# Kernel tuning notes

Measured on AMD Instinct MI355X. Metric: run time of the kernel, lower is better.

The kernel has to match this reference:

```python
import jax, jax.numpy as jnp
import numpy as np

TEMPERATURE = 0.07


def _unit(k, shape):
    x = jax.random.normal(k, shape, dtype=jnp.float32)
    return x / jnp.linalg.norm(x, axis=-1, keepdims=True)


def setup_inputs() -> dict:
    key = jax.random.key(0)
    ks = jax.random.split(key, 7)
    B, Cml, Cmc, D = 8192, 2048, 1000, 512
    features = _unit(ks[0], (B, D))
    ml_text = _unit(ks[1], (Cml, D))
    mc_text = _unit(ks[2], (Cmc, D))
    multilabel_targets = (jax.random.uniform(ks[3], (B, Cml)) < 0.05).astype(jnp.float32)
    # one-hot multiclass targets
    mc_idx = jax.random.randint(ks[4], (B,), 0, Cmc)
    multiclass_targets = jax.nn.one_hot(mc_idx, Cmc, dtype=jnp.float32)
    dataset_indices = jax.random.randint(ks[5], (B,), 0, 2).astype(jnp.int32)
    ratios = jax.random.uniform(ks[6], (Cml,), minval=0.05, maxval=0.95, dtype=jnp.float32)
    return {
        "features": features,
        "multilabel_text_features": ml_text,
        "multiclass_text_features": mc_text,
        "multilabel_targets": multilabel_targets,
        "multiclass_targets": multiclass_targets,
        "dataset_indices": dataset_indices,
        "ratios": ratios,
    }


def iterate_M(sim_matrix, b, num_iterations=2):
    # sim_matrix: [B, C, 2]; b: [C, 2]
    P = jnp.exp(sim_matrix)
    for _ in range(num_iterations):
        P = P / P.sum(axis=2, keepdims=True)          # row (last-dim) normalize
        P = P / (P.sum(axis=0) / b)                   # column normalize to marginals b
    return P


def iterate_P(sim_matrix, m, num_iterations=5):
    # sim_matrix: [B, C]
    P = jnp.exp(sim_matrix)
    for _ in range(num_iterations):
        row_sums = P.sum(axis=1)
        P = P / jnp.maximum(row_sums, 1.0)[:, None]
        P = P * m / P.sum()
    return P


def reference(features, multilabel_text_features, multiclass_text_features,
              multilabel_targets, multiclass_targets, dataset_indices, ratios):
    ml_sim = features @ multilabel_text_features.T / TEMPERATURE   # [B, Cml]
    mc_sim = features @ multiclass_text_features.T / TEMPERATURE   # [B, Cmc]

    n_mc = jnp.sum(dataset_indices == 1).astype(jnp.float32)
    n_ml = jnp.sum(dataset_indices == 0).astype(jnp.float32)
    m = n_mc + n_ml * 0.1

    P = iterate_P(mc_sim, m, 5)

    bs = ml_sim.shape[0]
    sim3 = jnp.stack([ml_sim / 2, -ml_sim / 2], axis=-1)           # [B, Cml, 2]
    b = jnp.stack([ratios, 1.0 - ratios], axis=1) * bs             # [Cml, 2]
    M = iterate_M(sim3, b, 2)

    ml_targets_final = jnp.stack([multilabel_targets, 1.0 - multilabel_targets], axis=-1)
    multilabel_loss = -jnp.sum(ml_targets_final * jnp.log(M)) * 0.5
    multiclass_loss = -jnp.sum(multiclass_targets * jnp.log(P))
    total_loss = multiclass_loss + multilabel_loss
    return total_loss
```

## Files before the change

kernel.cpp:

```cpp
#include <hip/hip_runtime.h>

typedef unsigned short u16;
typedef float f32x4 __attribute__((ext_vector_type(4)));
typedef short s16x8 __attribute__((ext_vector_type(8)));

#define GPTR(x) ((const __attribute__((address_space(1))) void*)(x))
#define LPTR(x) ((__attribute__((address_space(3))) void*)(x))

__device__ __forceinline__ u16 f32_to_bf16(float f) {
  unsigned u = __builtin_bit_cast(unsigned, f);
  u += 0x7FFFu + ((u >> 16) & 1u);
  return (u16)(u >> 16);
}
__device__ __forceinline__ float bf16_to_f32(u16 h) {
  unsigned u = ((unsigned)h) << 16;
  return __builtin_bit_cast(float, u);
}

__global__ __launch_bounds__(256) void k_cvt_all(
    const float* __restrict__ A, const float* __restrict__ ML, const float* __restrict__ MC,
    u16* __restrict__ Abf, u16* __restrict__ Bbf)
{
  int i = blockIdx.x * 256 + threadIdx.x;
  const float* src; u16* dst; int idx;
  bool pad = false;
  if (i < 1048576) { src = A; dst = Abf; idx = i; }
  else {
    int j = i - 1048576;
    if (j >= 393216) return;
    int row = j >> 7;
    dst = Bbf; idx = j;
    if (row < 2048) { src = ML; }
    else {
      int mcrow = row - 2048;
      src = MC; idx = j - 2048 * 128;
      pad = (mcrow >= 1000);
    }
  }
  ushort4 o = {0, 0, 0, 0};
  if (!pad) {
    float4 v = reinterpret_cast<const float4*>(src)[idx];
    o.x = f32_to_bf16(v.x); o.y = f32_to_bf16(v.y);
    o.z = f32_to_bf16(v.z); o.w = f32_to_bf16(v.w);
  }
  reinterpret_cast<ushort4*>(dst)[idx] = o;
}

__global__ __launch_bounds__(512) void k_gemm_fused(
    const u16* __restrict__ A, const u16* __restrict__ B,
    u16* __restrict__ Sml, float* __restrict__ colpart, float* __restrict__ pexp,
    float scale)
{
  constexpr int K = 512;
  constexpr int BK = 64;
  __shared__ __align__(16) u16 As[2][128 * BK];
  __shared__ __align__(16) u16 Bs[2][128 * BK];
  __shared__ float sred[128 * 4];

  const int tid  = threadIdx.x;
  const int lane = tid & 63;
  const int wave = tid >> 6;
  const int wr = wave >> 2;
  const int wc = wave & 3;

  int wg = (blockIdx.x & 7) * 192 + (blockIdx.x >> 3);
  const int bm = wg / 24;
  const int bn = wg % 24;
  const int row0 = bm * 128;
  const int col0 = bn * 128;
  const bool is_ml = (bn < 16);

  const int cr = (lane >> 4) * 4;
  const int cc = lane & 15;

  if (tid < 128) sred[tid] = 0.f;

  f32x4 acc[4][2];
#pragma unroll
  for (int i = 0; i < 4; ++i)
#pragma unroll
    for (int j = 0; j < 2; ++j) acc[i][j] = (f32x4){0.f, 0.f, 0.f, 0.f};

  auto stage = [&](int buf, int k0) {
#pragma unroll
    for (int q = 0; q < 2; ++q) {
      int base = wave * 128 + q * 64;
      int slot = base + lane;
      int r = slot >> 3, s = slot & 7;
      int sg = s ^ (r & 7);
      __builtin_amdgcn_global_load_lds(GPTR(A + (size_t)(row0 + r) * K + k0 + sg * 8),
                                       LPTR(&As[buf][base * 8]), 16, 0, 0);
      __builtin_amdgcn_global_load_lds(GPTR(B + (size_t)(col0 + r) * K + k0 + sg * 8),
                                       LPTR(&Bs[buf][base * 8]), 16, 0, 0);
    }
  };

  stage(0, 0);
  for (int t = 0; t < 8; ++t) {
    const int cur = t & 1;
    __syncthreads();
    if (t < 7) stage(cur ^ 1, (t + 1) * BK);
#pragma unroll
    for (int ks = 0; ks < 2; ++ks) {
      s16x8 af[4], bf[2];
#pragma unroll
      for (int mm = 0; mm < 4; ++mm) {
        int r = wr * 64 + mm * 16 + (lane & 15);
        int ss = (ks * 4 + (lane >> 4)) ^ (r & 7);
        af[mm] = *reinterpret_cast<const s16x8*>(&As[cur][r * BK + ss * 8]);
      }
#pragma unroll
      for (int nn = 0; nn < 2; ++nn) {
        int r = wc * 32 + nn * 16 + (lane & 15);
        int ss = (ks * 4 + (lane >> 4)) ^ (r & 7);
        bf[nn] = *reinterpret_cast<const s16x8*>(&Bs[cur][r * BK + ss * 8]);
      }
      __builtin_amdgcn_s_setprio(1);
#pragma unroll
      for (int mm = 0; mm < 4; ++mm)
#pragma unroll
        for (int nn = 0; nn < 2; ++nn)
          acc[mm][nn] = __builtin_amdgcn_mfma_f32_16x16x32_bf16(af[mm], bf[nn], acc[mm][nn], 0, 0, 0);
      __builtin_amdgcn_s_setprio(0);
    }
  }

  if (is_ml) {
#pragma unroll
    for (int mm = 0; mm < 4; ++mm) {
      int orow = row0 + wr * 64 + mm * 16 + cr;
#pragma unroll
      for (int nn = 0; nn < 2; ++nn) {
        int ocol = col0 + wc * 32 + nn * 16 + cc;
#pragma unroll
        for (int r = 0; r < 4; ++r)
          Sml[(size_t)(orow + r) * 2048 + ocol] = f32_to_bf16(acc[mm][nn][r] * scale);
      }
    }
    __syncthreads();
#pragma unroll
    for (int nn = 0; nn < 2; ++nn) {
      float cs = 0.f;
#pragma unroll
      for (int mm = 0; mm < 4; ++mm)
#pragma unroll
        for (int r = 0; r < 4; ++r) {
          float s = acc[mm][nn][r] * scale;
          cs += 1.f / (1.f + __expf(-s));
        }
      cs += __shfl_xor(cs, 16);
      cs += __shfl_xor(cs, 32);
      if (lane < 16) atomicAdd(&sred[wc * 32 + nn * 16 + lane], cs);
    }
    __syncthreads();
    if (tid < 128) colpart[(size_t)bm * 2048 + col0 + tid] = sred[tid];
  } else {
    const int mccol0 = col0 - 2048;
    float ex[16];
#pragma unroll
    for (int mm = 0; mm < 4; ++mm)
#pragma unroll
      for (int r = 0; r < 4; ++r) {
        float e = 0.f;
#pragma unroll
        for (int nn = 0; nn < 2; ++nn) {
          int ocol = mccol0 + wc * 32 + nn * 16 + cc;
          float s = acc[mm][nn][r] * scale;
          if (ocol < 1000) e += __expf(s);
        }
        ex[mm * 4 + r] = e;
      }
#pragma unroll
    for (int o = 1; o < 16; o <<= 1)
#pragma unroll
      for (int q = 0; q < 16; ++q) ex[q] += __shfl_xor(ex[q], o);
    __syncthreads();
    if ((lane & 15) == 0) {
#pragma unroll
      for (int mm = 0; mm < 4; ++mm)
#pragma unroll
        for (int r = 0; r < 4; ++r) {
          int lrow = wr * 64 + mm * 16 + cr + r;
          sred[lrow * 4 + wc] = ex[mm * 4 + r];
        }
    }
    __syncthreads();
    if (tid < 128) {
      size_t o = (size_t)(bn - 16) * 8192 + row0 + tid;
      pexp[o] = sred[tid * 4] + sred[tid * 4 + 1] + sred[tid * 4 + 2] + sred[tid * 4 + 3];
    }
  }
}

__global__ __launch_bounds__(256) void k_misc(
    const float* __restrict__ part, const float* __restrict__ ratios, float* __restrict__ c,
    const float* __restrict__ T2, const u16* __restrict__ A, const u16* __restrict__ B,
    float* __restrict__ rowdot, const float* __restrict__ pexp, float* __restrict__ Rbuf,
    float scale)
{
  if (blockIdx.x < 8) {
    int j = blockIdx.x * 256 + threadIdx.x;
    float s = 0.f;
    for (int ch = 0; ch < 64; ++ch) s += part[ch * 2048 + j];
    float b0 = ratios[j] * 8192.f;
    float b1 = (1.f - ratios[j]) * 8192.f;
    c[2 * j]     = b0 / s;
    c[2 * j + 1] = b1 / (8192.f - s);
    return;
  }
  if (blockIdx.x >= 2056) {
    int i = (blockIdx.x - 2056) * 256 + threadIdx.x;
    float e = 0.f;
#pragma unroll
    for (int ch = 0; ch < 8; ++ch) e += pexp[(size_t)ch * 8192 + i];
    Rbuf[i] = e;
    return;
  }
  int wave = threadIdx.x >> 6, lane = threadIdx.x & 63;
  int row = (blockIdx.x - 8) * 4 + wave;
  const float4* t4 = reinterpret_cast<const float4*>(T2 + (size_t)row * 1000);
  int idx = -1;
#pragma unroll
  for (int g = 0; g < 4; ++g) {
    int j4 = lane + g * 64;
    if (j4 < 250) {
      float4 v = t4[j4];
      if (v.x > 0.5f) idx = j4 * 4;
      if (v.y > 0.5f) idx = j4 * 4 + 1;
      if (v.z > 0.5f) idx = j4 * 4 + 2;
      if (v.w > 0.5f) idx = j4 * 4 + 3;
    }
  }
#pragma unroll
  for (int o = 32; o; o >>= 1) idx = max(idx, __shfl_xor(idx, o));

  s16x8 va = *reinterpret_cast<const s16x8*>(A + (size_t)row * 512 + lane * 8);
  s16x8 vb = *reinterpret_cast<const s16x8*>(B + (size_t)(2048 + idx) * 512 + lane * 8);
  float d = 0.f;
#pragma unroll
  for (int k = 0; k < 8; ++k)
    d += bf16_to_f32((u16)va[k]) * bf16_to_f32((u16)vb[k]);
#pragma unroll
  for (int o = 32; o; o >>= 1) d += __shfl_xor(d, o);
  if (lane == 0) rowdot[row] = d * scale;
}

__global__ __launch_bounds__(256) void k_ml_pass2(
    const u16* __restrict__ S, const float* __restrict__ T, const float* __restrict__ c,
    float* __restrict__ part2, float* __restrict__ partT, float* __restrict__ partE)
{
  const int t = threadIdx.x;
  const int r0 = blockIdx.x * 8;
  float c0[8], c1[8];
#pragma unroll
  for (int q = 0; q < 4; ++q) {
    float4 cv = reinterpret_cast<const float4*>(c)[t * 4 + q];
    c0[q * 2]     = cv.x; c1[q * 2]     = cv.y;
    c0[q * 2 + 1] = cv.z; c1[q * 2 + 1] = cv.w;
  }

  float q0s[8], ts[8];
#pragma unroll
  for (int k = 0; k < 8; ++k) { q0s[k] = 0.f; ts[k] = 0.f; }
  float tss = 0.f, ldsum = 0.f;

#pragma unroll 2
  for (int r = 0; r < 8; ++r) {
    size_t row = r0 + r;
    s16x8 sv = *reinterpret_cast<const s16x8*>(S + row * 2048 + t * 8);
    float4 ta = reinterpret_cast<const float4*>(T + row * 2048)[t * 2];
    float4 tb = reinterpret_cast<const float4*>(T + row * 2048)[t * 2 + 1];
    float tv[8] = {ta.x, ta.y, ta.z, ta.w, tb.x, tb.y, tb.z, tb.w};
#pragma unroll
    for (int k = 0; k < 8; ++k) {
      float s = bf16_to_f32((u16)sv[k]);
      float e = __expf(s);
      float n0 = e * c0[k];
      float den = n0 + c1[k];
      q0s[k] += n0 * __builtin_amdgcn_rcpf(den);
      ldsum  += __logf(den);
      ts[k]  += tv[k];
      tss    += tv[k] * s;
    }
  }
  float es = tss - ldsum;
#pragma unroll
  for (int k = 0; k < 8; ++k)
    es += __logf(c0[k] / c1[k]) * ts[k] + 8.f * __logf(c1[k]);

  float* p2 = part2 + (size_t)blockIdx.x * 2048 + t * 8;
  float* pT = partT + (size_t)blockIdx.x * 2048 + t * 8;
#pragma unroll
  for (int q = 0; q < 2; ++q) {
    reinterpret_cast<float4*>(p2)[q] = (float4){q0s[q*4], q0s[q*4+1], q0s[q*4+2], q0s[q*4+3]};
    reinterpret_cast<float4*>(pT)[q] = (float4){ts[q*4], ts[q*4+1], ts[q*4+2], ts[q*4+3]};
  }

  __shared__ float red[256];
  red[t] = es;
  __syncthreads();
  for (int o = 128; o; o >>= 1) {
    if (t < o) red[t] += red[t + o];
    __syncthreads();
  }
  if (t == 0) partE[blockIdx.x] = red[0];
}

__global__ __launch_bounds__(256) void k_colredA(
    const float* __restrict__ part2, const float* __restrict__ partT,
    float* __restrict__ pA2, float* __restrict__ pAT)
{
  int j = blockIdx.x * 256 + threadIdx.x;
  int ch0 = blockIdx.y * 16;
  float cs2 = 0.f, Tj = 0.f;
  for (int ch = ch0; ch < ch0 + 16; ++ch) {
    cs2 += part2[(size_t)ch * 2048 + j];
    Tj  += partT[(size_t)ch * 2048 + j];
  }
  pA2[(size_t)blockIdx.y * 2048 + j] = cs2;
  pAT[(size_t)blockIdx.y * 2048 + j] = Tj;
}

__global__ __launch_bounds__(256) void k_colredB(
    const float* __restrict__ pA2, const float* __restrict__ pAT,
    const float* __restrict__ ratios, float* __restrict__ partCol)
{
  int j = blockIdx.x * 256 + threadIdx.x;
  float cs2 = 0.f, Tj = 0.f;
  for (int ch = 0; ch < 64; ++ch) {
    cs2 += pA2[(size_t)ch * 2048 + j];
    Tj  += pAT[(size_t)ch * 2048 + j];
  }
  float b0 = ratios[j] * 8192.f;
  float b1 = (1.f - ratios[j]) * 8192.f;
  float colp = Tj * __logf(b0 / cs2) + (8192.f - Tj) * __logf(b1 / (8192.f - cs2));
  __shared__ float red[256];
  red[threadIdx.x] = colp;
  __syncthreads();
  for (int o = 128; o; o >>= 1) {
    if (threadIdx.x < o) red[threadIdx.x] += red[threadIdx.x + o];
    __syncthreads();
  }
  if (threadIdx.x == 0) partCol[blockIdx.x] = red[0];
}

__global__ __launch_bounds__(1024) void k_finalize(
    const float* __restrict__ Rbuf, const float* __restrict__ rowdot,
    const int* __restrict__ ds, const float* __restrict__ partE,
    const float* __restrict__ partCol, float* __restrict__ out)
{
  __shared__ float red[1024];
  const int tid = threadIdx.x;

  auto bsum = [&](float v) -> float {
    __syncthreads();
    red[tid] = v;
    __syncthreads();
    for (int o = 512; o; o >>= 1) {
      if (tid < o) red[tid] += red[tid + o];
      __syncthreads();
    }
    return red[0];
  };

  float nmc = 0.f, nml = 0.f;
  for (int i = tid; i < 8192; i += 1024) {
    int d = ds[i];
    nmc += (d == 1) ? 1.f : 0.f;
    nml += (d == 0) ? 1.f : 0.f;
  }
  float n_mc = bsum(nmc);
  float n_ml = bsum(nml);
  float m = n_mc + 0.1f * n_ml;

  float a[8], Rv[8], rdv[8];
#pragma unroll
  for (int q = 0; q < 8; ++q) {
    int i = tid + q * 1024;
    Rv[q] = Rbuf[i]; rdv[q] = rowdot[i]; a[q] = 1.f;
  }
  for (int it = 0; it < 5; ++it) {
    float p = 0.f;
#pragma unroll
    for (int q = 0; q < 8; ++q) {
      a[q] = a[q] / fmaxf(Rv[q] * a[q], 1.f);
      p += Rv[q] * a[q];
    }
    float tot = bsum(p);
    float sc = m / tot;
#pragma unroll
    for (int q = 0; q < 8; ++q) a[q] *= sc;
  }
  float mcp = 0.f;
#pragma unroll
  for (int q = 0; q < 8; ++q)
    mcp += rdv[q] + __logf(a[q]);

  float ep = partE[tid];
  float cp = (tid < 8) ? partCol[tid] : 0.f;

  float total = bsum(-mcp - 0.5f * (cp + ep));
  if (tid == 0) out[0] = total;
}

extern "C" void kernel_launch(void* const* d_in, const int* in_sizes, int n_in,
                              void* d_out, int out_size, void* d_ws, size_t ws_size,
                              hipStream_t stream)
{
  const float* features = (const float*)d_in[0];
  const float* ml_text  = (const float*)d_in[1];
  const float* mc_text  = (const float*)d_in[2];
  const float* ml_tgt   = (const float*)d_in[3];
  const float* mc_tgt   = (const float*)d_in[4];
  const int*   dsidx    = (const int*)d_in[5];
  const float* ratios   = (const float*)d_in[6];
  float* out = (float*)d_out;

  char* ws = (char*)d_ws;
  size_t off = 0;
  auto alloc = [&](size_t bytes) -> void* {
    void* p = ws + off;
    off += (bytes + 255) & ~(size_t)255;
    return p;
  };
  u16*   Abf    = (u16*)alloc((size_t)8192 * 512 * 2);
  u16*   Bbf    = (u16*)alloc((size_t)3072 * 512 * 2);
  u16*   Sml    = (u16*)alloc((size_t)8192 * 2048 * 2);
  float* part1  = (float*)alloc((size_t)64 * 2048 * 4);
  float* cbuf   = (float*)alloc((size_t)2048 * 2 * 4);
  float* part2  = (float*)alloc((size_t)1024 * 2048 * 4);
  float* partT  = (float*)alloc((size_t)1024 * 2048 * 4);
  float* pA2    = (float*)alloc((size_t)64 * 2048 * 4);
  float* pAT    = (float*)alloc((size_t)64 * 2048 * 4);
  float* partE  = (float*)alloc((size_t)1024 * 4);
  float* partCol= (float*)alloc((size_t)8 * 4);
  float* pexp   = (float*)alloc((size_t)8 * 8192 * 4);
  float* Rbuf   = (float*)alloc((size_t)8192 * 4);
  float* rowdot = (float*)alloc((size_t)8192 * 4);

  k_cvt_all<<<(1441792 + 255) / 256, 256, 0, stream>>>(features, ml_text, mc_text, Abf, Bbf);

  const float scale = 1.0f / 0.07f;
  k_gemm_fused<<<1536, 512, 0, stream>>>(Abf, Bbf, Sml, part1, pexp, scale);

  k_misc<<<2088, 256, 0, stream>>>(part1, ratios, cbuf, mc_tgt, Abf, Bbf, rowdot, pexp, Rbuf, scale);
  k_ml_pass2<<<1024, 256, 0, stream>>>(Sml, ml_tgt, cbuf, part2, partT, partE);
  k_colredA<<<dim3(8, 64), 256, 0, stream>>>(part2, partT, pA2, pAT);
  k_colredB<<<8, 256, 0, stream>>>(pA2, pAT, ratios, partCol);
  k_finalize<<<1, 1024, 0, stream>>>(Rbuf, rowdot, dsidx, partE, partCol, out);
}
```

Baseline: 110.5 us.

## Enlarge fused GEMM tile to 256x256 with interleaved LDS staging

The fused similarity GEMM grows its output tile from 128x128 to 256x256, so each wave computes an 8x4 grid of MFMA tiles instead of 4x2. Each A/B element loaded from global memory is now reused across more of the output, and the grid drops from 1536 to 384 blocks. The K loop is restructured so the next tile's global-to-LDS loads are issued in chunks between the MFMA phases, with explicit barriers and waitcnts. In exchange the kernel uses much more LDS (64KB of staging) and far more accumulator registers. With only 384 blocks, the grid gives roughly 1.5 waves over the CUs, which risks tail imbalance; downstream partial-sum counts are halved to match.

```diff
diff --git a/kernel.cpp b/kernel.cpp
--- a/kernel.cpp
+++ b/kernel.cpp
@@ -46,16 +46,16 @@
   reinterpret_cast<ushort4*>(dst)[idx] = o;
 }
 
-__global__ __launch_bounds__(512) void k_gemm_fused(
+__global__ __launch_bounds__(512, 2) void k_gemm_fused(
     const u16* __restrict__ A, const u16* __restrict__ B,
     u16* __restrict__ Sml, float* __restrict__ colpart, float* __restrict__ pexp,
     float scale)
 {
   constexpr int K = 512;
   constexpr int BK = 64;
-  __shared__ __align__(16) u16 As[2][128 * BK];
-  __shared__ __align__(16) u16 Bs[2][128 * BK];
-  __shared__ float sred[128 * 4];
+  __shared__ __align__(16) u16 As[2][256 * BK];
+  __shared__ __align__(16) u16 Bs[2][256 * BK];
+  __shared__ float sred[1024];
 
   const int tid  = threadIdx.x;
   const int lane = tid & 63;
@@ -63,86 +63,111 @@
   const int wr = wave >> 2;
   const int wc = wave & 3;
 
-  int wg = (blockIdx.x & 7) * 192 + (blockIdx.x >> 3);
-  const int bm = wg / 24;
-  const int bn = wg % 24;
-  const int row0 = bm * 128;
-  const int col0 = bn * 128;
-  const bool is_ml = (bn < 16);
+  int wg = (blockIdx.x & 7) * 48 + (blockIdx.x >> 3);
+  const int bm = wg / 12;
+  const int bn = wg % 12;
+  const int row0 = bm * 256;
+  const int col0 = bn * 256;
+  const bool is_ml = (bn < 8);
 
   const int cr = (lane >> 4) * 4;
   const int cc = lane & 15;
 
-  if (tid < 128) sred[tid] = 0.f;
-
-  f32x4 acc[4][2];
-#pragma unroll
-  for (int i = 0; i < 4; ++i)
-#pragma unroll
-    for (int j = 0; j < 2; ++j) acc[i][j] = (f32x4){0.f, 0.f, 0.f, 0.f};
-
-  auto stage = [&](int buf, int k0) {
-#pragma unroll
-    for (int q = 0; q < 2; ++q) {
-      int base = wave * 128 + q * 64;
-      int slot = base + lane;
-      int r = slot >> 3, s = slot & 7;
-      int sg = s ^ (r & 7);
-      __builtin_amdgcn_global_load_lds(GPTR(A + (size_t)(row0 + r) * K + k0 + sg * 8),
-                                       LPTR(&As[buf][base * 8]), 16, 0, 0);
-      __builtin_amdgcn_global_load_lds(GPTR(B + (size_t)(col0 + r) * K + k0 + sg * 8),
-                                       LPTR(&Bs[buf][base * 8]), 16, 0, 0);
-    }
+  f32x4 acc[8][4];
+#pragma unroll
+  for (int i = 0; i < 8; ++i)
+#pragma unroll
+    for (int j = 0; j < 4; ++j) acc[i][j] = (f32x4){0.f, 0.f, 0.f, 0.f};
+
+  const u16* Agp[4]; const u16* Bgp[4]; int stb[4];
+#pragma unroll
+  for (int q = 0; q < 4; ++q) {
+    int base = wave * 256 + q * 64;
+    int slot = base + lane;
+    int r = slot >> 3, s = slot & 7;
+    int sg = s ^ (r & 7);
+    stb[q] = base;
+    Agp[q] = A + (size_t)(row0 + r) * K + sg * 8;
+    Bgp[q] = B + (size_t)(col0 + r) * K + sg * 8;
+  }
+  auto stage_pair = [&](int buf, int k0, int q) {
+    __builtin_amdgcn_global_load_lds(GPTR(Agp[q] + k0), LPTR(&As[buf][stb[q] * 8]), 16, 0, 0);
+    __builtin_amdgcn_global_load_lds(GPTR(Bgp[q] + k0), LPTR(&Bs[buf][stb[q] * 8]), 16, 0, 0);
   };
 
-  stage(0, 0);
-  for (int t = 0; t < 8; ++t) {
-    const int cur = t & 1;
-    __syncthreads();
-    if (t < 7) stage(cur ^ 1, (t + 1) * BK);
-#pragma unroll
-    for (int ks = 0; ks < 2; ++ks) {
-      s16x8 af[4], bf[2];
-#pragma unroll
-      for (int mm = 0; mm < 4; ++mm) {
-        int r = wr * 64 + mm * 16 + (lane & 15);
-        int ss = (ks * 4 + (lane >> 4)) ^ (r & 7);
-        af[mm] = *reinterpret_cast<const s16x8*>(&As[cur][r * BK + ss * 8]);
+#pragma unroll
+  for (int q = 0; q < 4; ++q) stage_pair(0, 0, q);
+
+#pragma unroll
+  for (int kt = 0; kt < 8; ++kt) {
+    const int cur = kt & 1;
+    const int knext = (kt + 1) * BK;
+    asm volatile("s_waitcnt vmcnt(0)" ::: "memory");
+    __builtin_amdgcn_sched_barrier(0);
+    __builtin_amdgcn_s_barrier();
+
+    s16x8 bf[4][2];
+#pragma unroll
+    for (int p = 0; p < 4; ++p) {
+      if (p == 0) {
+#pragma unroll
+        for (int nn = 0; nn < 4; ++nn)
+#pragma unroll
+          for (int ks = 0; ks < 2; ++ks) {
+            int rc = wc * 64 + nn * 16 + (lane & 15);
+            int ss = (ks * 4 + (lane >> 4)) ^ (rc & 7);
+            bf[nn][ks] = *reinterpret_cast<const s16x8*>(&Bs[cur][rc * BK + ss * 8]);
+          }
       }
-#pragma unroll
-      for (int nn = 0; nn < 2; ++nn) {
-        int r = wc * 32 + nn * 16 + (lane & 15);
-        int ss = (ks * 4 + (lane >> 4)) ^ (r & 7);
-        bf[nn] = *reinterpret_cast<const s16x8*>(&Bs[cur][r * BK + ss * 8]);
+      s16x8 af[2][2];
+#pragma unroll
+      for (int mm2 = 0; mm2 < 2; ++mm2)
+#pragma unroll
+        for (int ks = 0; ks < 2; ++ks) {
+          int rr = wr * 128 + (p * 2 + mm2) * 16 + (lane & 15);
+          int ss = (ks * 4 + (lane >> 4)) ^ (rr & 7);
+          af[mm2][ks] = *reinterpret_cast<const s16x8*>(&As[cur][rr * BK + ss * 8]);
+        }
+      if (kt < 7 && p < 2) {
+        stage_pair(cur ^ 1, knext, p * 2);
+        stage_pair(cur ^ 1, knext, p * 2 + 1);
       }
+      __builtin_amdgcn_s_barrier();
+      asm volatile("s_waitcnt lgkmcnt(0)" ::: "memory");
+      __builtin_amdgcn_sched_barrier(0);
       __builtin_amdgcn_s_setprio(1);
 #pragma unroll
-      for (int mm = 0; mm < 4; ++mm)
-#pragma unroll
-        for (int nn = 0; nn < 2; ++nn)
-          acc[mm][nn] = __builtin_amdgcn_mfma_f32_16x16x32_bf16(af[mm], bf[nn], acc[mm][nn], 0, 0, 0);
+      for (int mm2 = 0; mm2 < 2; ++mm2)
+#pragma unroll
+        for (int nn = 0; nn < 4; ++nn)
+#pragma unroll
+          for (int ks = 0; ks < 2; ++ks)
+            acc[p * 2 + mm2][nn] = __builtin_amdgcn_mfma_f32_16x16x32_bf16(
+                af[mm2][ks], bf[nn][ks], acc[p * 2 + mm2][nn], 0, 0, 0);
       __builtin_amdgcn_s_setprio(0);
+      __builtin_amdgcn_s_barrier();
     }
   }
 
   if (is_ml) {
 #pragma unroll
-    for (int mm = 0; mm < 4; ++mm) {
-      int orow = row0 + wr * 64 + mm * 16 + cr;
-#pragma unroll
-      for (int nn = 0; nn < 2; ++nn) {
-        int ocol = col0 + wc * 32 + nn * 16 + cc;
+    for (int mm = 0; mm < 8; ++mm) {
+      int orow = row0 + wr * 128 + mm * 16 + cr;
+#pragma unroll
+      for (int nn = 0; nn < 4; ++nn) {
+        int ocol = col0 + wc * 64 + nn * 16 + cc;
 #pragma unroll
         for (int r = 0; r < 4; ++r)
           Sml[(size_t)(orow + r) * 2048 + ocol] = f32_to_bf16(acc[mm][nn][r] * scale);
       }
     }
-    __syncthreads();
-#pragma unroll
-    for (int nn = 0; nn < 2; ++nn) {
+    if (tid < 256) sred[tid] = 0.f;
+    __syncthreads();
+#pragma unroll
+    for (int nn = 0; nn < 4; ++nn) {
       float cs = 0.f;
 #pragma unroll
-      for (int mm = 0; mm < 4; ++mm)
+      for (int mm = 0; mm < 8; ++mm)
 #pragma unroll
         for (int r = 0; r < 4; ++r) {
           float s = acc[mm][nn][r] * scale;
@@ -150,43 +175,41 @@
         }
       cs += __shfl_xor(cs, 16);
       cs += __shfl_xor(cs, 32);
-      if (lane < 16) atomicAdd(&sred[wc * 32 + nn * 16 + lane], cs);
-    }
-    __syncthreads();
-    if (tid < 128) colpart[(size_t)bm * 2048 + col0 + tid] = sred[tid];
+      if (lane < 16) atomicAdd(&sred[wc * 64 + nn * 16 + lane], cs);
+    }
+    __syncthreads();
+    if (tid < 256) colpart[(size_t)bm * 2048 + col0 + tid] = sred[tid];
   } else {
     const int mccol0 = col0 - 2048;
-    float ex[16];
-#pragma unroll
-    for (int mm = 0; mm < 4; ++mm)
+#pragma unroll
+    for (int mm = 0; mm < 8; ++mm) {
+      float ex[4];
 #pragma unroll
       for (int r = 0; r < 4; ++r) {
         float e = 0.f;
 #pragma unroll
-        for (int nn = 0; nn < 2; ++nn) {
-          int ocol = mccol0 + wc * 32 + nn * 16 + cc;
+        for (int nn = 0; nn < 4; ++nn) {
+          int ocol = mccol0 + wc * 64 + nn * 16 + cc;
           float s = acc[mm][nn][r] * scale;
           if (ocol < 1000) e += __expf(s);
         }
-        ex[mm * 4 + r] = e;
+        ex[r] = e;
       }
 #pragma unroll
-    for (int o = 1; o < 16; o <<= 1)
-#pragma unroll
-      for (int q = 0; q < 16; ++q) ex[q] += __shfl_xor(ex[q], o);
-    __syncthreads();
-    if ((lane & 15) == 0) {
-#pragma unroll
-      for (int mm = 0; mm < 4; ++mm)
+      for (int o = 1; o < 16; o <<= 1)
+#pragma unroll
+        for (int r = 0; r < 4; ++r) ex[r] += __shfl_xor(ex[r], o);
+      if ((lane & 15) == 0) {
 #pragma unroll
         for (int r = 0; r < 4; ++r) {
-          int lrow = wr * 64 + mm * 16 + cr + r;
-          sred[lrow * 4 + wc] = ex[mm * 4 + r];
+          int lrow = wr * 128 + mm * 16 + cr + r;
+          sred[lrow * 4 + wc] = ex[r];
         }
-    }
-    __syncthreads();
-    if (tid < 128) {
-      size_t o = (size_t)(bn - 16) * 8192 + row0 + tid;
+      }
+    }
+    __syncthreads();
+    if (tid < 256) {
+      size_t o = (size_t)(bn - 8) * 8192 + row0 + tid;
       pexp[o] = sred[tid * 4] + sred[tid * 4 + 1] + sred[tid * 4 + 2] + sred[tid * 4 + 3];
     }
   }
@@ -201,7 +224,7 @@
   if (blockIdx.x < 8) {
     int j = blockIdx.x * 256 + threadIdx.x;
     float s = 0.f;
-    for (int ch = 0; ch < 64; ++ch) s += part[ch * 2048 + j];
+    for (int ch = 0; ch < 32; ++ch) s += part[ch * 2048 + j];
     float b0 = ratios[j] * 8192.f;
     float b1 = (1.f - ratios[j]) * 8192.f;
     c[2 * j]     = b0 / s;
@@ -212,7 +235,7 @@
     int i = (blockIdx.x - 2056) * 256 + threadIdx.x;
     float e = 0.f;
 #pragma unroll
-    for (int ch = 0; ch < 8; ++ch) e += pexp[(size_t)ch * 8192 + i];
+    for (int ch = 0; ch < 4; ++ch) e += pexp[(size_t)ch * 8192 + i];
     Rbuf[i] = e;
     return;
   }
@@ -426,7 +449,7 @@
   u16*   Abf    = (u16*)alloc((size_t)8192 * 512 * 2);
   u16*   Bbf    = (u16*)alloc((size_t)3072 * 512 * 2);
   u16*   Sml    = (u16*)alloc((size_t)8192 * 2048 * 2);
-  float* part1  = (float*)alloc((size_t)64 * 2048 * 4);
+  float* part1  = (float*)alloc((size_t)32 * 2048 * 4);
   float* cbuf   = (float*)alloc((size_t)2048 * 2 * 4);
   float* part2  = (float*)alloc((size_t)1024 * 2048 * 4);
   float* partT  = (float*)alloc((size_t)1024 * 2048 * 4);
@@ -434,14 +457,14 @@
   float* pAT    = (float*)alloc((size_t)64 * 2048 * 4);
   float* partE  = (float*)alloc((size_t)1024 * 4);
   float* partCol= (float*)alloc((size_t)8 * 4);
-  float* pexp   = (float*)alloc((size_t)8 * 8192 * 4);
+  float* pexp   = (float*)alloc((size_t)4 * 8192 * 4);
   float* Rbuf   = (float*)alloc((size_t)8192 * 4);
   float* rowdot = (float*)alloc((size_t)8192 * 4);
 
   k_cvt_all<<<(1441792 + 255) / 256, 256, 0, stream>>>(features, ml_text, mc_text, Abf, Bbf);
 
   const float scale = 1.0f / 0.07f;
-  k_gemm_fused<<<1536, 512, 0, stream>>>(Abf, Bbf, Sml, part1, pexp, scale);
+  k_gemm_fused<<<384, 512, 0, stream>>>(Abf, Bbf, Sml, part1, pexp, scale);
 
   k_misc<<<2088, 256, 0, stream>>>(part1, ratios, cbuf, mc_tgt, Abf, Bbf, rowdot, pexp, Rbuf, scale);
   k_ml_pass2<<<1024, 256, 0, stream>>>(Sml, ml_tgt, cbuf, part2, partT, partE);
```

Measured after the change: 123.5 us. +11.7%, slower.
